# Kernel tuning notes

Hardware: AMD Instinct MI355X
Metric: run time of the kernel (lower is better)

## Reference

```python
import jax, jax.numpy as jnp
import numpy as np
from math import sqrt


def _attention(q, k, v, scale):
    # q: [B, L, H, E], k: [B, S, H, E], v: [B, S, H, D]
    scores = jnp.einsum('blhe,bshe->bhls', q, k)
    A = jax.nn.softmax(scale * scores, axis=-1)           # [B, H, L, S]
    V = jnp.einsum('bhls,bshd->blhd', A, v)               # [B, L, H, D]
    B, L, H, D = V.shape
    return V.reshape(B, L, H * D)


def setup_inputs() -> dict:
    key = jax.random.key(0)
    ks = jax.random.split(key, 6)
    shape = (4, 2048, 8, 64)  # [B, L, H, E]
    names = ['queries_w', 'keys_w', 'values_w', 'queries_m', 'keys_m', 'values_m']
    inp = {n: jax.random.normal(k, shape, dtype=jnp.float32) for n, k in zip(names, ks)}
    inp['attn_mask'] = jnp.zeros((1,), dtype=bool)  # unused by the module
    return inp


def reference(queries_w, keys_w, values_w, queries_m, keys_m, values_m, attn_mask):
    E = queries_w.shape[-1]
    scale = 1.0 / sqrt(E)
    c0 = _attention(queries_w, keys_w, values_w, scale)   # w -> w
    c1 = _attention(queries_m, keys_m, values_m, scale)   # m -> m
    c2 = _attention(queries_w, keys_m, values_m, scale)   # w -> m
    c3 = _attention(queries_m, keys_w, values_w, scale)   # m -> w
    return (c0, c1, c2, c3)
```

## Files before the change

kernel.cpp:

```cpp
#include <hip/hip_runtime.h>


typedef _Float16 half8 __attribute__((ext_vector_type(8)));
typedef _Float16 half4 __attribute__((ext_vector_type(4)));
typedef _Float16 half2t __attribute__((ext_vector_type(2)));
typedef float f32x4 __attribute__((ext_vector_type(4)));

#define MFMA_QK(a, b, c) __builtin_amdgcn_mfma_f32_16x16x32_f16(a, b, c, 0, 0, 0)
#define MFMA_PV(a, b, c) __builtin_amdgcn_mfma_f32_16x16x16f16(a, b, c, 0, 0, 0)

static __device__ inline half2t pk(float a, float b) {
    return __builtin_bit_cast(half2t, __builtin_amdgcn_cvt_pkrtz(a, b));
}

static __device__ __forceinline__ void gload_lds16(const _Float16* g, _Float16* l) {
    __builtin_amdgcn_global_load_lds(
        (const __attribute__((address_space(1))) unsigned int*)g,
        (__attribute__((address_space(3))) unsigned int*)l, 16, 0, 0);
}

#define QSCALE 0.1803368867f

#define TENS_ELEMS 4194304

__global__ __launch_bounds__(256) void prep_kernel(
    const float* __restrict__ kw, const float* __restrict__ km,
    const float* __restrict__ vw, const float* __restrict__ vm,
    _Float16* __restrict__ wsK, _Float16* __restrict__ wsV)
{
    const int t = blockIdx.x, bh = blockIdx.y, z = blockIdx.z;
    const int set = z & 1;
    const int b = bh >> 3, h = bh & 7;
    const int tid = threadIdx.x;
    const size_t headOff = ((size_t)b * 2048) * 512 + (size_t)h * 64;
    const size_t tileOff = ((((size_t)set * 32 + bh) * 32) + t) * 4096;

    __shared__ _Float16 T[64 * 68];

    if (z < 2) {
        const float* kb = (set ? km : kw) + headOff;
        _Float16* dst = wsK + tileOff;
#pragma unroll
        for (int w = 0; w < 2; ++w) {
            const int c = tid + w * 256;
            const int l16 = c & 15, q = (c >> 4) & 3, kc = (c >> 6) & 1, nb = (c >> 7) & 3;
            const float* p = kb + (size_t)(t * 64 + nb * 16 + l16) * 512 + kc * 32 + q * 8;
            float4 x = *(const float4*)p;
            float4 y = *(const float4*)(p + 4);
            half2t h0 = pk(x.x * QSCALE, x.y * QSCALE), h1 = pk(x.z * QSCALE, x.w * QSCALE);
            half2t h2 = pk(y.x * QSCALE, y.y * QSCALE), h3 = pk(y.z * QSCALE, y.w * QSCALE);
            half8 o = {h0.x, h0.y, h1.x, h1.y, h2.x, h2.y, h3.x, h3.y};
            *(half8*)(dst + (size_t)c * 8) = o;
        }
    } else {
        const float* vb = (set ? vm : vw) + headOff;
        const int s_row = tid >> 2, cg = (tid & 3) * 16;
        const float* row = vb + (size_t)(t * 64 + s_row) * 512 + cg;
#pragma unroll
        for (int k4 = 0; k4 < 4; ++k4) {
            float4 v = *(const float4*)(row + k4 * 4);
            const int d0 = cg + k4 * 4;
            T[(d0 + 0) * 68 + s_row] = (_Float16)v.x;
            T[(d0 + 1) * 68 + s_row] = (_Float16)v.y;
            T[(d0 + 2) * 68 + s_row] = (_Float16)v.z;
            T[(d0 + 3) * 68 + s_row] = (_Float16)v.w;
        }
        __syncthreads();
        _Float16* dst = wsV + tileOff;
#pragma unroll
        for (int w = 0; w < 2; ++w) {
            const int c = tid + w * 256;
            const int lane = c & 63, db = (c >> 6) & 3, m = (c >> 8) & 1;
            const int l16 = lane & 15, q = lane >> 4;
            const _Float16* tp = &T[(db * 16 + l16) * 68 + m * 32 + q * 4];
            half4 a = *(const half4*)tp;
            half4 b2 = *(const half4*)(tp + 16);
            half8 o = {a[0], a[1], a[2], a[3], b2[0], b2[1], b2[2], b2[3]};
            *(half8*)(dst + (size_t)c * 8) = o;
        }
    }
}

__global__ __launch_bounds__(256, 4) void bm_attn_main(
    const float* __restrict__ qw, const float* __restrict__ qm,
    const _Float16* __restrict__ wsK, const _Float16* __restrict__ wsV,
    float* __restrict__ out)
{
    const int ltile = blockIdx.x, bh = blockIdx.y, set = blockIdx.z;
    const int b = bh >> 3, h = bh & 7;
    const float* Q0 = set ? qm : qw;
    const float* Q1 = set ? qw : qm;
    const int c0 = set ? 1 : 0, c1 = set ? 2 : 3;

    const int tid = threadIdx.x;
    const int wave = tid >> 6, lane = tid & 63;
    const int quad = lane >> 4, l16 = lane & 15;

    __shared__ __align__(16) _Float16 ldsK[2][4096];
    __shared__ __align__(16) _Float16 ldsV[2][4096];

    const size_t headOff = ((size_t)b * 2048) * 512 + (size_t)h * 64;
    const size_t tileBase = (((size_t)set * 32 + bh) * 32) * 4096;
    const _Float16* tK = wsK + tileBase;
    const _Float16* tV = wsV + tileBase;

    const int rowBase = ltile * 64 + wave * 16;
    half8 qB[2][2];
    {
        const float* qs[2] = { Q0 + headOff, Q1 + headOff };
#pragma unroll
        for (int s = 0; s < 2; ++s)
#pragma unroll
            for (int kc = 0; kc < 2; ++kc) {
                const float* p = qs[s] + (size_t)(rowBase + l16) * 512 + kc * 32 + quad * 8;
                float4 x = *(const float4*)p;
                float4 y = *(const float4*)(p + 4);
                half2t h0 = pk(x.x, x.y), h1 = pk(x.z, x.w);
                half2t h2 = pk(y.x, y.y), h3 = pk(y.z, y.w);
                qB[s][kc] = (half8){h0.x, h0.y, h1.x, h1.y, h2.x, h2.y, h3.x, h3.y};
            }
    }

    f32x4 accO[2][4];
    f32x4 rsD[2];
#pragma unroll
    for (int s = 0; s < 2; ++s) {
        rsD[s] = (f32x4){0.f, 0.f, 0.f, 0.f};
#pragma unroll
        for (int d = 0; d < 4; ++d) accO[s][d] = (f32x4){0.f, 0.f, 0.f, 0.f};
    }
    const half8 ones8 = {(_Float16)1.f, (_Float16)1.f, (_Float16)1.f, (_Float16)1.f,
                         (_Float16)1.f, (_Float16)1.f, (_Float16)1.f, (_Float16)1.f};

    auto stage = [&](int t, int buf) {
        const _Float16* gK = tK + (size_t)t * 4096 + tid * 8;
        const _Float16* gV = tV + (size_t)t * 4096 + tid * 8;
        _Float16* lK = &ldsK[buf][wave * 512];
        _Float16* lV = &ldsV[buf][wave * 512];
        gload_lds16(gK, lK);
        gload_lds16(gK + 2048, lK + 2048);
        gload_lds16(gV, lV);
        gload_lds16(gV + 2048, lV + 2048);
    };

    stage(0, 0);
    __syncthreads();
    int cur = 0;

#pragma unroll 1
    for (int tile = 0; tile < 32; ++tile) {
        if (tile + 1 < 32) stage(tile + 1, cur ^ 1);

        const _Float16* kt = &ldsK[cur][lane * 8];
        const _Float16* vt = &ldsV[cur][lane * 8];
#pragma unroll
        for (int m = 0; m < 2; ++m) {
            const _Float16* kb0 = kt + (m * 4) * 512;
            half8 k00 = *(const half8*)(kb0 + 0 * 512);
            half8 k01 = *(const half8*)(kb0 + 1 * 512);
            half8 k10 = *(const half8*)(kb0 + 2 * 512);
            half8 k11 = *(const half8*)(kb0 + 3 * 512);
            f32x4 z = {0.f, 0.f, 0.f, 0.f};
            f32x4 s00 = MFMA_QK(k00, qB[0][0], z);
            s00 = MFMA_QK(k01, qB[0][1], s00);
            f32x4 s01 = MFMA_QK(k10, qB[0][0], z);
            s01 = MFMA_QK(k11, qB[0][1], s01);
            f32x4 s10 = MFMA_QK(k00, qB[1][0], z);
            s10 = MFMA_QK(k01, qB[1][1], s10);
            f32x4 s11 = MFMA_QK(k10, qB[1][0], z);
            s11 = MFMA_QK(k11, qB[1][1], s11);

            half2t a0 = pk(__builtin_amdgcn_exp2f(s00[0]), __builtin_amdgcn_exp2f(s00[1]));
            half2t a1 = pk(__builtin_amdgcn_exp2f(s00[2]), __builtin_amdgcn_exp2f(s00[3]));
            half2t a2 = pk(__builtin_amdgcn_exp2f(s01[0]), __builtin_amdgcn_exp2f(s01[1]));
            half2t a3 = pk(__builtin_amdgcn_exp2f(s01[2]), __builtin_amdgcn_exp2f(s01[3]));
            half8 pa0 = {a0.x, a0.y, a1.x, a1.y, a2.x, a2.y, a3.x, a3.y};
            half2t b0 = pk(__builtin_amdgcn_exp2f(s10[0]), __builtin_amdgcn_exp2f(s10[1]));
            half2t b1 = pk(__builtin_amdgcn_exp2f(s10[2]), __builtin_amdgcn_exp2f(s10[3]));
            half2t b2 = pk(__builtin_amdgcn_exp2f(s11[0]), __builtin_amdgcn_exp2f(s11[1]));
            half2t b3 = pk(__builtin_amdgcn_exp2f(s11[2]), __builtin_amdgcn_exp2f(s11[3]));
            half8 pa1 = {b0.x, b0.y, b1.x, b1.y, b2.x, b2.y, b3.x, b3.y};

            rsD[0] = MFMA_QK(pa0, ones8, rsD[0]);
            rsD[1] = MFMA_QK(pa1, ones8, rsD[1]);

            const _Float16* vb0 = vt + (m * 4) * 512;
#pragma unroll
            for (int db = 0; db < 4; ++db) {
                half8 bv = *(const half8*)(vb0 + db * 512);
                accO[0][db] = MFMA_QK(pa0, bv, accO[0][db]);
                accO[1][db] = MFMA_QK(pa1, bv, accO[1][db]);
            }
        }
        __syncthreads();
        cur ^= 1;
    }

#pragma unroll
    for (int s = 0; s < 2; ++s) {
        const int c = (s == 0) ? c0 : c1;
        float* ob = out + (size_t)c * TENS_ELEMS + headOff;
#pragma unroll
        for (int r = 0; r < 4; ++r) {
            const float inv = 1.0f / rsD[s][r];
            const int row = rowBase + quad * 4 + r;
#pragma unroll
            for (int db = 0; db < 4; ++db) {
                ob[(size_t)row * 512 + db * 16 + l16] = accO[s][db][r] * inv;
            }
        }
    }
}

__global__ __launch_bounds__(256) void bm_attn_fallback(
    const float* __restrict__ qw, const float* __restrict__ kw, const float* __restrict__ vw,
    const float* __restrict__ qm, const float* __restrict__ km, const float* __restrict__ vm,
    float* __restrict__ out)
{
    const int ltile = blockIdx.x, bh = blockIdx.y, set = blockIdx.z;
    const int b = bh >> 3, h = bh & 7;
    const float* Q0 = set ? qm : qw;
    const float* Q1 = set ? qw : qm;
    const int c0 = set ? 1 : 0, c1 = set ? 2 : 3;
    const int tid = threadIdx.x;
    const int wave = tid >> 6, lane = tid & 63;
    const int quad = lane >> 4, l16 = lane & 15;
    __shared__ __align__(16) _Float16 Kt[64 * 72];
    __shared__ __align__(16) _Float16 Vt[64 * 72];
    const size_t headOff = ((size_t)b * 2048) * 512 + (size_t)h * 64;
    const float* kb = (set ? km : kw) + headOff;
    const float* vb = (set ? vm : vw) + headOff;
    const int rowBase = ltile * 64 + wave * 16;
    half8 qB[2][2];
    {
        const float* qs[2] = { Q0 + headOff, Q1 + headOff };
#pragma unroll
        for (int s = 0; s < 2; ++s)
#pragma unroll
            for (int kc = 0; kc < 2; ++kc) {
                const float* p = qs[s] + (size_t)(rowBase + l16) * 512 + kc * 32 + quad * 8;
                half8 q;
#pragma unroll
                for (int j = 0; j < 8; ++j) q[j] = (_Float16)(p[j] * QSCALE);
                qB[s][kc] = q;
            }
    }
    f32x4 accO[2][4];
#pragma unroll
    for (int s = 0; s < 2; ++s)
#pragma unroll
        for (int d = 0; d < 4; ++d) accO[s][d] = (f32x4){0.f, 0.f, 0.f, 0.f};
    float rs0 = 0.f, rs1 = 0.f;
#pragma unroll 1
    for (int tile = 0; tile < 32; ++tile) {
        const int s0 = tile * 64;
        __syncthreads();
        {
            const int r0 = tid >> 4, f4 = (tid & 15) * 4;
#pragma unroll
            for (int p4 = 0; p4 < 4; ++p4) {
                const int row = p4 * 16 + r0;
                float4 v = *(const float4*)(kb + (size_t)(s0 + row) * 512 + f4);
                half2t a = pk(v.x, v.y), b2 = pk(v.z, v.w);
                half4 o = {a.x, a.y, b2.x, b2.y};
                *(half4*)&Kt[row * 72 + f4] = o;
            }
            const int sl = tid & 63, dq = tid >> 6;
            const float* vrow = vb + (size_t)(s0 + sl) * 512;
#pragma unroll
            for (int i = 0; i < 4; ++i) {
                const int d0 = dq * 16 + i * 4;
                float4 v = *(const float4*)(vrow + d0);
                Vt[(d0 + 0) * 72 + sl] = (_Float16)v.x;
                Vt[(d0 + 1) * 72 + sl] = (_Float16)v.y;
                Vt[(d0 + 2) * 72 + sl] = (_Float16)v.z;
                Vt[(d0 + 3) * 72 + sl] = (_Float16)v.w;
            }
        }
        __syncthreads();
#pragma unroll
        for (int nb = 0; nb < 4; ++nb) {
            half8 k0 = *(const half8*)&Kt[(nb * 16 + l16) * 72 + quad * 8];
            half8 k1 = *(const half8*)&Kt[(nb * 16 + l16) * 72 + 32 + quad * 8];
            f32x4 z = {0.f, 0.f, 0.f, 0.f};
            f32x4 st0 = MFMA_QK(k0, qB[0][0], z);
            st0 = MFMA_QK(k1, qB[0][1], st0);
            f32x4 st1 = MFMA_QK(k0, qB[1][0], z);
            st1 = MFMA_QK(k1, qB[1][1], st1);
            half2t p00 = pk(__builtin_amdgcn_exp2f(st0[0]), __builtin_amdgcn_exp2f(st0[1]));
            half2t p01 = pk(__builtin_amdgcn_exp2f(st0[2]), __builtin_amdgcn_exp2f(st0[3]));
            half2t p10 = pk(__builtin_amdgcn_exp2f(st1[0]), __builtin_amdgcn_exp2f(st1[1]));
            half2t p11 = pk(__builtin_amdgcn_exp2f(st1[2]), __builtin_amdgcn_exp2f(st1[3]));
            rs0 += (float)p00.x + (float)p00.y + (float)p01.x + (float)p01.y;
            rs1 += (float)p10.x + (float)p10.y + (float)p11.x + (float)p11.y;
            half4 ph0 = {p00.x, p00.y, p01.x, p01.y};
            half4 ph1 = {p10.x, p10.y, p11.x, p11.y};
#pragma unroll
            for (int db = 0; db < 4; ++db) {
                half4 bv = *(const half4*)&Vt[(db * 16 + l16) * 72 + nb * 16 + quad * 4];
                accO[0][db] = MFMA_PV(ph0, bv, accO[0][db]);
                accO[1][db] = MFMA_PV(ph1, bv, accO[1][db]);
            }
        }
    }
#pragma unroll
    for (int s = 0; s < 2; ++s) {
        float rs = (s == 0) ? rs0 : rs1;
        rs += __shfl_xor(rs, 16);
        rs += __shfl_xor(rs, 32);
        const float inv = 1.0f / rs;
        const int c = (s == 0) ? c0 : c1;
        float* ob = out + (size_t)c * TENS_ELEMS + headOff;
#pragma unroll
        for (int r = 0; r < 4; ++r) {
            const float invr = __shfl(inv, quad * 4 + r);
            const int row = rowBase + quad * 4 + r;
#pragma unroll
            for (int db = 0; db < 4; ++db) {
                ob[(size_t)row * 512 + db * 16 + l16] = accO[s][db][r] * invr;
            }
        }
    }
}

extern "C" void kernel_launch(void* const* d_in, const int* in_sizes, int n_in,
                              void* d_out, int out_size, void* d_ws, size_t ws_size,
                              hipStream_t stream) {
    const float* qw = (const float*)d_in[0];
    const float* kw = (const float*)d_in[1];
    const float* vw = (const float*)d_in[2];
    const float* qm = (const float*)d_in[3];
    const float* km = (const float*)d_in[4];
    const float* vm = (const float*)d_in[5];
    float* out = (float*)d_out;

    dim3 block(256);
    const size_t NEED = (size_t)4 * TENS_ELEMS * sizeof(_Float16);

    if (ws_size >= NEED) {
        _Float16* wsK = (_Float16*)d_ws;
        _Float16* wsV = wsK + (size_t)2 * TENS_ELEMS;
        prep_kernel<<<dim3(32, 32, 4), block, 0, stream>>>(kw, km, vw, vm, wsK, wsV);
        bm_attn_main<<<dim3(32, 32, 2), block, 0, stream>>>(qw, qm, wsK, wsV, out);
    } else {
        bm_attn_fallback<<<dim3(32, 32, 2), block, 0, stream>>>(qw, kw, vw, qm, km, vm, out);
    }
}
```

Measured before the change: 277.2 us.

## Double query rows per block, remap blocks across XCDs, coalesce prep loads

The main attention kernel now has each wave handle 32 query rows instead of 16, so each K/V tile staged in LDS is reused across twice as many MFMAs and the grid is halved. Block indices are remapped so consecutive work items spread across the XCDs in an interleaved way, with blocks sharing a head likely co-located for L2 reuse. The prep kernel reads K and V rows with coalesced float4 loads through LDS before reordering them. In exchange, register pressure roughly doubles for the accumulators, and occupancy is lowered via launch bounds 3, which may reduce latency hiding.

```diff
diff --git a/kernel.cpp b/kernel.cpp
--- a/kernel.cpp
+++ b/kernel.cpp
@@ -34,36 +34,40 @@
     const int tid = threadIdx.x;
     const size_t headOff = ((size_t)b * 2048) * 512 + (size_t)h * 64;
     const size_t tileOff = ((((size_t)set * 32 + bh) * 32) + t) * 4096;
-
-    __shared__ _Float16 T[64 * 68];
+    const int lr = tid >> 4, lc = (tid & 15) * 4;
 
     if (z < 2) {
-        const float* kb = (set ? km : kw) + headOff;
+        __shared__ _Float16 T[64 * 72];
+        const float* kb = (set ? km : kw) + headOff + (size_t)t * 64 * 512;
+#pragma unroll
+        for (int i = 0; i < 4; ++i) {
+            const int row = i * 16 + lr;
+            float4 v = *(const float4*)(kb + (size_t)row * 512 + lc);
+            half2t h0 = pk(v.x * QSCALE, v.y * QSCALE);
+            half2t h1 = pk(v.z * QSCALE, v.w * QSCALE);
+            half4 o = {h0.x, h0.y, h1.x, h1.y};
+            *(half4*)&T[row * 72 + lc] = o;
+        }
+        __syncthreads();
         _Float16* dst = wsK + tileOff;
 #pragma unroll
         for (int w = 0; w < 2; ++w) {
             const int c = tid + w * 256;
             const int l16 = c & 15, q = (c >> 4) & 3, kc = (c >> 6) & 1, nb = (c >> 7) & 3;
-            const float* p = kb + (size_t)(t * 64 + nb * 16 + l16) * 512 + kc * 32 + q * 8;
-            float4 x = *(const float4*)p;
-            float4 y = *(const float4*)(p + 4);
-            half2t h0 = pk(x.x * QSCALE, x.y * QSCALE), h1 = pk(x.z * QSCALE, x.w * QSCALE);
-            half2t h2 = pk(y.x * QSCALE, y.y * QSCALE), h3 = pk(y.z * QSCALE, y.w * QSCALE);
-            half8 o = {h0.x, h0.y, h1.x, h1.y, h2.x, h2.y, h3.x, h3.y};
+            half8 o = *(const half8*)&T[(nb * 16 + l16) * 72 + kc * 32 + q * 8];
             *(half8*)(dst + (size_t)c * 8) = o;
         }
     } else {
-        const float* vb = (set ? vm : vw) + headOff;
-        const int s_row = tid >> 2, cg = (tid & 3) * 16;
-        const float* row = vb + (size_t)(t * 64 + s_row) * 512 + cg;
-#pragma unroll
-        for (int k4 = 0; k4 < 4; ++k4) {
-            float4 v = *(const float4*)(row + k4 * 4);
-            const int d0 = cg + k4 * 4;
-            T[(d0 + 0) * 68 + s_row] = (_Float16)v.x;
-            T[(d0 + 1) * 68 + s_row] = (_Float16)v.y;
-            T[(d0 + 2) * 68 + s_row] = (_Float16)v.z;
-            T[(d0 + 3) * 68 + s_row] = (_Float16)v.w;
+        __shared__ _Float16 Tv[64 * 76];
+        const float* vb = (set ? vm : vw) + headOff + (size_t)t * 64 * 512;
+#pragma unroll
+        for (int i = 0; i < 4; ++i) {
+            const int row = i * 16 + lr;
+            float4 v = *(const float4*)(vb + (size_t)row * 512 + lc);
+            Tv[(lc + 0) * 76 + row] = (_Float16)v.x;
+            Tv[(lc + 1) * 76 + row] = (_Float16)v.y;
+            Tv[(lc + 2) * 76 + row] = (_Float16)v.z;
+            Tv[(lc + 3) * 76 + row] = (_Float16)v.w;
         }
         __syncthreads();
         _Float16* dst = wsV + tileOff;
@@ -72,7 +76,7 @@
             const int c = tid + w * 256;
             const int lane = c & 63, db = (c >> 6) & 3, m = (c >> 8) & 1;
             const int l16 = lane & 15, q = lane >> 4;
-            const _Float16* tp = &T[(db * 16 + l16) * 68 + m * 32 + q * 4];
+            const _Float16* tp = &Tv[(db * 16 + l16) * 76 + m * 32 + q * 4];
             half4 a = *(const half4*)tp;
             half4 b2 = *(const half4*)(tp + 16);
             half8 o = {a[0], a[1], a[2], a[3], b2[0], b2[1], b2[2], b2[3]};
@@ -81,12 +85,15 @@
     }
 }
 
-__global__ __launch_bounds__(256, 4) void bm_attn_main(
+__global__ __launch_bounds__(256, 3) void bm_attn_main(
     const float* __restrict__ qw, const float* __restrict__ qm,
     const _Float16* __restrict__ wsK, const _Float16* __restrict__ wsV,
     float* __restrict__ out)
 {
-    const int ltile = blockIdx.x, bh = blockIdx.y, set = blockIdx.z;
+    const int hw = (int)blockIdx.x + 16 * (int)blockIdx.y + 512 * (int)blockIdx.z;
+    const int work = (hw & 7) * 128 + (hw >> 3);
+    const int ltile = work & 15, bh = (work >> 4) & 31, set = work >> 9;
+
     const int b = bh >> 3, h = bh & 7;
     const float* Q0 = set ? qm : qw;
     const float* Q1 = set ? qw : qm;
@@ -104,31 +111,35 @@
     const _Float16* tK = wsK + tileBase;
     const _Float16* tV = wsV + tileBase;
 
-    const int rowBase = ltile * 64 + wave * 16;
-    half8 qB[2][2];
+    const int rowBase = ltile * 128 + wave * 32;
+    half8 qB[2][2][2];
     {
         const float* qs[2] = { Q0 + headOff, Q1 + headOff };
 #pragma unroll
         for (int s = 0; s < 2; ++s)
 #pragma unroll
-            for (int kc = 0; kc < 2; ++kc) {
-                const float* p = qs[s] + (size_t)(rowBase + l16) * 512 + kc * 32 + quad * 8;
-                float4 x = *(const float4*)p;
-                float4 y = *(const float4*)(p + 4);
-                half2t h0 = pk(x.x, x.y), h1 = pk(x.z, x.w);
-                half2t h2 = pk(y.x, y.y), h3 = pk(y.z, y.w);
-                qB[s][kc] = (half8){h0.x, h0.y, h1.x, h1.y, h2.x, h2.y, h3.x, h3.y};
-            }
-    }
-
-    f32x4 accO[2][4];
-    f32x4 rsD[2];
-#pragma unroll
-    for (int s = 0; s < 2; ++s) {
-        rsD[s] = (f32x4){0.f, 0.f, 0.f, 0.f};
-#pragma unroll
-        for (int d = 0; d < 4; ++d) accO[s][d] = (f32x4){0.f, 0.f, 0.f, 0.f};
-    }
+            for (int rb = 0; rb < 2; ++rb)
+#pragma unroll
+                for (int kc = 0; kc < 2; ++kc) {
+                    const float* p = qs[s] + (size_t)(rowBase + rb * 16 + l16) * 512 + kc * 32 + quad * 8;
+                    float4 x = *(const float4*)p;
+                    float4 y = *(const float4*)(p + 4);
+                    half2t h0 = pk(x.x, x.y), h1 = pk(x.z, x.w);
+                    half2t h2 = pk(y.x, y.y), h3 = pk(y.z, y.w);
+                    qB[s][rb][kc] = (half8){h0.x, h0.y, h1.x, h1.y, h2.x, h2.y, h3.x, h3.y};
+                }
+    }
+
+    f32x4 accO[2][2][4];
+    f32x4 rsD[2][2];
+#pragma unroll
+    for (int s = 0; s < 2; ++s)
+#pragma unroll
+        for (int rb = 0; rb < 2; ++rb) {
+            rsD[s][rb] = (f32x4){0.f, 0.f, 0.f, 0.f};
+#pragma unroll
+            for (int d = 0; d < 4; ++d) accO[s][rb][d] = (f32x4){0.f, 0.f, 0.f, 0.f};
+        }
     const half8 ones8 = {(_Float16)1.f, (_Float16)1.f, (_Float16)1.f, (_Float16)1.f,
                          (_Float16)1.f, (_Float16)1.f, (_Float16)1.f, (_Float16)1.f};
 
@@ -155,41 +166,38 @@
         const _Float16* vt = &ldsV[cur][lane * 8];
 #pragma unroll
         for (int m = 0; m < 2; ++m) {
-            const _Float16* kb0 = kt + (m * 4) * 512;
-            half8 k00 = *(const half8*)(kb0 + 0 * 512);
-            half8 k01 = *(const half8*)(kb0 + 1 * 512);
-            half8 k10 = *(const half8*)(kb0 + 2 * 512);
-            half8 k11 = *(const half8*)(kb0 + 3 * 512);
-            f32x4 z = {0.f, 0.f, 0.f, 0.f};
-            f32x4 s00 = MFMA_QK(k00, qB[0][0], z);
-            s00 = MFMA_QK(k01, qB[0][1], s00);
-            f32x4 s01 = MFMA_QK(k10, qB[0][0], z);
-            s01 = MFMA_QK(k11, qB[0][1], s01);
-            f32x4 s10 = MFMA_QK(k00, qB[1][0], z);
-            s10 = MFMA_QK(k01, qB[1][1], s10);
-            f32x4 s11 = MFMA_QK(k10, qB[1][0], z);
-            s11 = MFMA_QK(k11, qB[1][1], s11);
-
-            half2t a0 = pk(__builtin_amdgcn_exp2f(s00[0]), __builtin_amdgcn_exp2f(s00[1]));
-            half2t a1 = pk(__builtin_amdgcn_exp2f(s00[2]), __builtin_amdgcn_exp2f(s00[3]));
-            half2t a2 = pk(__builtin_amdgcn_exp2f(s01[0]), __builtin_amdgcn_exp2f(s01[1]));
-            half2t a3 = pk(__builtin_amdgcn_exp2f(s01[2]), __builtin_amdgcn_exp2f(s01[3]));
-            half8 pa0 = {a0.x, a0.y, a1.x, a1.y, a2.x, a2.y, a3.x, a3.y};
-            half2t b0 = pk(__builtin_amdgcn_exp2f(s10[0]), __builtin_amdgcn_exp2f(s10[1]));
-            half2t b1 = pk(__builtin_amdgcn_exp2f(s10[2]), __builtin_amdgcn_exp2f(s10[3]));
-            half2t b2 = pk(__builtin_amdgcn_exp2f(s11[0]), __builtin_amdgcn_exp2f(s11[1]));
-            half2t b3 = pk(__builtin_amdgcn_exp2f(s11[2]), __builtin_amdgcn_exp2f(s11[3]));
-            half8 pa1 = {b0.x, b0.y, b1.x, b1.y, b2.x, b2.y, b3.x, b3.y};
-
-            rsD[0] = MFMA_QK(pa0, ones8, rsD[0]);
-            rsD[1] = MFMA_QK(pa1, ones8, rsD[1]);
-
-            const _Float16* vb0 = vt + (m * 4) * 512;
+            half8 k00 = *(const half8*)(kt + (m * 4 + 0) * 512);
+            half8 k01 = *(const half8*)(kt + (m * 4 + 1) * 512);
+            half8 k10 = *(const half8*)(kt + (m * 4 + 2) * 512);
+            half8 k11 = *(const half8*)(kt + (m * 4 + 3) * 512);
+
+            half8 pa[2][2];
+#pragma unroll
+            for (int s = 0; s < 2; ++s)
+#pragma unroll
+                for (int rb = 0; rb < 2; ++rb) {
+                    f32x4 z4 = {0.f, 0.f, 0.f, 0.f};
+                    f32x4 slo = MFMA_QK(k00, qB[s][rb][0], z4);
+                    slo = MFMA_QK(k01, qB[s][rb][1], slo);
+                    f32x4 shi = MFMA_QK(k10, qB[s][rb][0], z4);
+                    shi = MFMA_QK(k11, qB[s][rb][1], shi);
+
+                    half2t e0 = pk(__builtin_amdgcn_exp2f(slo[0]), __builtin_amdgcn_exp2f(slo[1]));
+                    half2t e1 = pk(__builtin_amdgcn_exp2f(slo[2]), __builtin_amdgcn_exp2f(slo[3]));
+                    half2t e2 = pk(__builtin_amdgcn_exp2f(shi[0]), __builtin_amdgcn_exp2f(shi[1]));
+                    half2t e3 = pk(__builtin_amdgcn_exp2f(shi[2]), __builtin_amdgcn_exp2f(shi[3]));
+                    half8 p8 = {e0.x, e0.y, e1.x, e1.y, e2.x, e2.y, e3.x, e3.y};
+                    pa[s][rb] = p8;
+                    rsD[s][rb] = MFMA_QK(p8, ones8, rsD[s][rb]);
+                }
+
 #pragma unroll
             for (int db = 0; db < 4; ++db) {
-                half8 bv = *(const half8*)(vb0 + db * 512);
-                accO[0][db] = MFMA_QK(pa0, bv, accO[0][db]);
-                accO[1][db] = MFMA_QK(pa1, bv, accO[1][db]);
+                half8 bv = *(const half8*)(vt + (m * 4 + db) * 512);
+                accO[0][0][db] = MFMA_QK(pa[0][0], bv, accO[0][0][db]);
+                accO[0][1][db] = MFMA_QK(pa[0][1], bv, accO[0][1][db]);
+                accO[1][0][db] = MFMA_QK(pa[1][0], bv, accO[1][0][db]);
+                accO[1][1][db] = MFMA_QK(pa[1][1], bv, accO[1][1][db]);
             }
         }
         __syncthreads();
@@ -201,14 +209,16 @@
         const int c = (s == 0) ? c0 : c1;
         float* ob = out + (size_t)c * TENS_ELEMS + headOff;
 #pragma unroll
-        for (int r = 0; r < 4; ++r) {
-            const float inv = 1.0f / rsD[s][r];
-            const int row = rowBase + quad * 4 + r;
-#pragma unroll
-            for (int db = 0; db < 4; ++db) {
-                ob[(size_t)row * 512 + db * 16 + l16] = accO[s][db][r] * inv;
-            }
-        }
+        for (int rb = 0; rb < 2; ++rb)
+#pragma unroll
+            for (int r = 0; r < 4; ++r) {
+                const float inv = 1.0f / rsD[s][rb][r];
+                const int row = rowBase + rb * 16 + quad * 4 + r;
+#pragma unroll
+                for (int db = 0; db < 4; ++db) {
+                    ob[(size_t)row * 512 + db * 16 + l16] = accO[s][rb][db][r] * inv;
+                }
+            }
     }
 }
 
@@ -341,7 +351,7 @@
         _Float16* wsK = (_Float16*)d_ws;
         _Float16* wsV = wsK + (size_t)2 * TENS_ELEMS;
         prep_kernel<<<dim3(32, 32, 4), block, 0, stream>>>(kw, km, vw, vm, wsK, wsV);
-        bm_attn_main<<<dim3(32, 32, 2), block, 0, stream>>>(qw, qm, wsK, wsV, out);
+        bm_attn_main<<<dim3(16, 32, 2), block, 0, stream>>>(qw, qm, wsK, wsV, out);
     } else {
         bm_attn_fallback<<<dim3(32, 32, 2), block, 0, stream>>>(qw, kw, vw, qm, km, vm, out);
     }
```

Measured after the change: 272.0 us. About the same (-1.9%).
